# Kernel optimization log

Hardware: AMD Instinct MI355X
Metric: run time of the kernel (lower is better)

## Reference

```python
import jax, jax.numpy as jnp
import numpy as np

C = 256; G = 8; K = 3; P = K * K; GC = C // G
PAD = K // 2; PAD_DW = 1
EPS_LN = 1e-5; EPS_DWLN = 1e-6; EPS_BN = 1e-5
OFFSET_SCALE = 1.0


def _ln(x, g, b, eps=EPS_LN):
    mu = x.mean(-1, keepdims=True)
    var = ((x - mu) ** 2).mean(-1, keepdims=True)
    return (x - mu) * jax.lax.rsqrt(var + eps) * g + b


def _bn(x, g, b, m, v):  # x: NCHW, eval-mode batchnorm with running stats
    s = jax.lax.rsqrt(v + EPS_BN)
    return (x - m[None, :, None, None]) * (g * s)[None, :, None, None] + b[None, :, None, None]


def _dcnv3_core(x, offset, mask):
    # x: (N,H,W,C) projected input; offset: (N,H,W,G*P*2); mask: (N,H,W,G,P) softmaxed
    N, H, W, _ = x.shape
    Hp, Wp = H + 2 * PAD, W + 2 * PAD
    x_pad = jnp.pad(x, ((0, 0), (PAD, PAD), (PAD, PAD), (0, 0)))
    img = x_pad.reshape(N, Hp, Wp, G, GC).transpose(0, 3, 4, 1, 2)  # (N,G,gc,Hp,Wp)
    # reference points, normalized by padded spatial dims (stride=1, dilation=1)
    start = (K - 1) // 2 + 0.5
    ref_x = (start + jnp.arange(W, dtype=x.dtype)) / Wp
    ref_y = (start + jnp.arange(H, dtype=x.dtype)) / Hp
    rx, ry = jnp.meshgrid(ref_x, ref_y, indexing='xy')  # (H,W)
    ref = jnp.stack([rx, ry], -1)  # (H,W,2) as (x,y)
    # dilation grid (kernel tap offsets), tap index p = i_w*K + j_h per torch meshgrid order
    gw = (jnp.arange(K, dtype=x.dtype) - (K - 1) // 2) / Wp
    gh = (jnp.arange(K, dtype=x.dtype) - (K - 1) // 2) / Hp
    gxx, gyy = jnp.meshgrid(gw, gh, indexing='ij')
    grid = jnp.stack([gxx, gyy], -1).reshape(P, 2)
    norm = jnp.array([Wp, Hp], dtype=x.dtype)
    off = offset.reshape(N, H, W, G, P, 2) * (OFFSET_SCALE / norm)
    loc = ref[None, :, :, None, None, :] + grid * OFFSET_SCALE + off  # (N,H,W,G,P,2)
    sg = (2.0 * loc - 1.0).transpose(0, 3, 1, 2, 4, 5).reshape(N, G, H * W, P, 2)

    def sample_one(im, gr):  # im: (gc,Hp,Wp), gr: (HW,P,2) in [-1,1]
        gx = (gr[..., 0] + 1.0) * (Wp / 2) - 0.5  # align_corners=False
        gy = (gr[..., 1] + 1.0) * (Hp / 2) - 0.5
        x0 = jnp.floor(gx); y0 = jnp.floor(gy)
        wx = gx - x0; wy = gy - y0
        def gat(ix, iy):
            valid = ((ix >= 0) & (ix <= Wp - 1) & (iy >= 0) & (iy <= Hp - 1)).astype(im.dtype)
            ixc = jnp.clip(ix, 0, Wp - 1).astype(jnp.int32)
            iyc = jnp.clip(iy, 0, Hp - 1).astype(jnp.int32)
            return im[:, iyc, ixc] * valid  # (gc,HW,P), zero padding outside
        return (gat(x0, y0) * ((1 - wx) * (1 - wy))
                + gat(x0 + 1, y0) * (wx * (1 - wy))
                + gat(x0, y0 + 1) * ((1 - wx) * wy)
                + gat(x0 + 1, y0 + 1) * (wx * wy))

    sampled = jax.vmap(jax.vmap(sample_one))(img, sg)  # (N,G,gc,HW,P)
    m = mask.transpose(0, 3, 1, 2, 4).reshape(N, G, 1, H * W, P)
    out = (sampled * m).sum(-1)  # (N,G,gc,HW)
    return out.transpose(0, 3, 1, 2).reshape(N, H, W, C)


def _dcnv3(inp, dw_w, dw_b, dwln_g, dwln_b, off_w, off_b, msk_w, msk_b, inp_w, inp_b, outp_w, outp_b):
    N, H, W, _ = inp.shape
    x = inp @ inp_w + inp_b  # input_proj
    # depthwise conv offset/mask branch (on the raw input, not the projection)
    x1 = jax.lax.conv_general_dilated(inp, dw_w, (1, 1), ((PAD_DW, PAD_DW), (PAD_DW, PAD_DW)),
                                      dimension_numbers=('NHWC', 'HWIO', 'NHWC'),
                                      feature_group_count=C) + dw_b
    x1 = jax.nn.gelu(_ln(x1, dwln_g, dwln_b, EPS_DWLN), approximate=False)
    offset = x1 @ off_w + off_b  # (N,H,W,G*P*2)
    mask = jax.nn.softmax((x1 @ msk_w + msk_b).reshape(N, H, W, G, P), axis=-1)
    return _dcnv3_core(x, offset, mask) @ outp_w + outp_b  # output_proj


def _forward(x, conv1_w, bn1_g, bn1_b, bn1_m, bn1_v, ln1_g, ln1_b, dw_w, dw_b, dwln_g, dwln_b,
             off_w, off_b, msk_w, msk_b, inp_w, inp_b, outp_w, outp_b, gamma1,
             ln2_g, ln2_b, fc1_w, fc1_b, fc2_w, fc2_b, gamma2, bn2_g, bn2_b, bn2_m, bn2_v):
    out = jax.lax.conv_general_dilated(x, conv1_w, (1, 1), ((1, 1), (1, 1)),
                                       dimension_numbers=('NCHW', 'OIHW', 'NCHW'))
    out = jax.nn.relu(_bn(out, bn1_g, bn1_b, bn1_m, bn1_v))
    t = out.transpose(0, 2, 3, 1)  # NHWC for the InternImage layer
    # post_norm InternImage layer with layer_scale
    d = _dcnv3(t, dw_w, dw_b, dwln_g, dwln_b, off_w, off_b, msk_w, msk_b, inp_w, inp_b, outp_w, outp_b)
    t = t + gamma1 * _ln(d, ln1_g, ln1_b)
    h = jax.nn.gelu(t @ fc1_w + fc1_b, approximate=False) @ fc2_w + fc2_b
    t = t + gamma2 * _ln(h, ln2_g, ln2_b)
    out = _bn(t.transpose(0, 3, 1, 2), bn2_g, bn2_b, bn2_m, bn2_v)
    return jax.nn.relu(out + x)  # residual (downsample is None: stride=1, inplanes==planes)


def setup_inputs() -> dict:
    key = jax.random.key(0)
    ks = iter(jax.random.split(key, 48))
    rn = lambda shape, s=1.0: jax.random.normal(next(ks), shape, dtype=jnp.float32) * s
    hid = 4 * C
    d = {}
    d['x'] = rn((8, C, 56, 56))
    d['conv1_w'] = rn((C, C, 3, 3), (2.0 / (9 * C)) ** 0.5)
    d['bn1_g'] = jnp.ones((C,), jnp.float32); d['bn1_b'] = jnp.zeros((C,), jnp.float32)
    d['bn1_m'] = rn((C,), 0.1)
    d['bn1_v'] = jax.random.uniform(next(ks), (C,), jnp.float32, 0.5, 1.5)
    d['ln1_g'] = jnp.ones((C,), jnp.float32); d['ln1_b'] = jnp.zeros((C,), jnp.float32)
    d['dw_w'] = rn((3, 3, 1, C), (1.0 / 9) ** 0.5); d['dw_b'] = jnp.zeros((C,), jnp.float32)
    d['dwln_g'] = jnp.ones((C,), jnp.float32); d['dwln_b'] = jnp.zeros((C,), jnp.float32)
    d['off_w'] = rn((C, G * P * 2), 0.01); d['off_b'] = rn((G * P * 2,), 0.01)
    d['msk_w'] = rn((C, G * P), 0.01); d['msk_b'] = jnp.zeros((G * P,), jnp.float32)
    d['inp_w'] = rn((C, C), C ** -0.5); d['inp_b'] = jnp.zeros((C,), jnp.float32)
    d['outp_w'] = rn((C, C), C ** -0.5); d['outp_b'] = jnp.zeros((C,), jnp.float32)
    d['gamma1'] = rn((C,), 0.01)
    d['ln2_g'] = jnp.ones((C,), jnp.float32); d['ln2_b'] = jnp.zeros((C,), jnp.float32)
    d['fc1_w'] = rn((C, hid), C ** -0.5); d['fc1_b'] = jnp.zeros((hid,), jnp.float32)
    d['fc2_w'] = rn((hid, C), hid ** -0.5); d['fc2_b'] = jnp.zeros((C,), jnp.float32)
    d['gamma2'] = rn((C,), 0.01)
    d['bn2_g'] = jnp.ones((C,), jnp.float32); d['bn2_b'] = jnp.zeros((C,), jnp.float32)
    d['bn2_m'] = rn((C,), 0.1)
    d['bn2_v'] = jax.random.uniform(next(ks), (C,), jnp.float32, 0.5, 1.5)
    return d


def reference(x, conv1_w, bn1_g, bn1_b, bn1_m, bn1_v, ln1_g, ln1_b, dw_w, dw_b, dwln_g, dwln_b,
              off_w, off_b, msk_w, msk_b, inp_w, inp_b, outp_w, outp_b, gamma1,
              ln2_g, ln2_b, fc1_w, fc1_b, fc2_w, fc2_b, gamma2, bn2_g, bn2_b, bn2_m, bn2_v):
    return _forward(x, conv1_w, bn1_g, bn1_b, bn1_m, bn1_v, ln1_g, ln1_b, dw_w, dw_b, dwln_g, dwln_b,
                    off_w, off_b, msk_w, msk_b, inp_w, inp_b, outp_w, outp_b, gamma1,
                    ln2_g, ln2_b, fc1_w, fc1_b, fc2_w, fc2_b, gamma2, bn2_g, bn2_b, bn2_m, bn2_v)
```

## Files before the change

### kernel.cpp

```cpp
#include <hip/hip_runtime.h>
#include <cmath>

#define N_   8
#define H_   56
#define W_   56
#define C_   256
#define HW_  3136
#define NHW_ 25088
#define G_   8
#define GC_  32
#define P_   9
#define HID_ 1024
#define XP_H 58
#define XP_W 58

typedef __attribute__((ext_vector_type(8))) short bf16x8;
typedef __attribute__((ext_vector_type(4))) float f32x4;

#define GLOAD_LDS16(g, l) __builtin_amdgcn_global_load_lds( \
    (const __attribute__((address_space(1))) void*)(g), \
    (__attribute__((address_space(3))) void*)(l), 16, 0, 0)

__device__ __forceinline__ unsigned short f2bf(float f) {
    unsigned u = __float_as_uint(f);
    u += 0x7FFF + ((u >> 16) & 1);
    return (unsigned short)(u >> 16);
}

__device__ __forceinline__ float gelu_exact(float v) {
    return 0.5f * v * (1.f + erff(v * 0.70710678118654752f));
}

__device__ __forceinline__ float2 block_sum2(float a, float b, float* sm) {
    int lane = threadIdx.x & 63;
    int wid  = threadIdx.x >> 6;
#pragma unroll
    for (int off = 32; off > 0; off >>= 1) {
        a += __shfl_down(a, off, 64);
        b += __shfl_down(b, off, 64);
    }
    if (lane == 0) { sm[wid] = a; sm[wid + 4] = b; }
    __syncthreads();
    float ra = sm[0] + sm[1] + sm[2] + sm[3];
    float rb = sm[4] + sm[5] + sm[6] + sm[7];
    __syncthreads();
    return make_float2(ra, rb);
}

__global__ __launch_bounds__(256) void k_prep_xpad(const float* __restrict__ x, unsigned short* __restrict__ xpad) {
    int nh = blockIdx.x;
    int n = nh / H_, h = nh - n * H_;
    int c = threadIdx.x;
    const float* xr = x + ((size_t)(n * C_ + c)) * HW_ + h * W_;
    unsigned short* orow = xpad + ((size_t)((n * XP_H + h + 1) * XP_W + 1)) * C_ + c;
    for (int w = 0; w < W_; ++w) orow[(size_t)w * C_] = f2bf(xr[w]);
}

__global__ __launch_bounds__(256) void k_prep_wTT(const float* __restrict__ w, unsigned short* __restrict__ wTT) {
    int i  = blockIdx.x * 256 + threadIdx.x;
    int ci = i & 255;
    int r  = i >> 8;
    int co = r & 255;
    int kk = r >> 8;
    wTT[i] = f2bf(w[(co * 256 + ci) * 9 + kk]);
}

__global__ __launch_bounds__(256) void k_prep_sqT(const float* __restrict__ src, unsigned short* __restrict__ dst) {
    int n = blockIdx.x, k = threadIdx.x;
    dst[n * C_ + k] = f2bf(src[k * C_ + n]);
}

__global__ __launch_bounds__(256) void k_prep_fc1T(const float* __restrict__ src, unsigned short* __restrict__ dst) {
    int n = blockIdx.x, k = threadIdx.x;
    dst[(size_t)n * C_ + k] = f2bf(src[(size_t)k * HID_ + n]);
}

__global__ __launch_bounds__(256) void k_prep_fc2T(const float* __restrict__ src, unsigned short* __restrict__ dst) {
    int n = blockIdx.x, k0 = threadIdx.x;
#pragma unroll
    for (int q = 0; q < 4; ++q) {
        int k = q * 256 + k0;
        dst[(size_t)n * HID_ + k] = f2bf(src[(size_t)k * C_ + n]);
    }
}

__global__ __launch_bounds__(256) void k_prep_om(const float* __restrict__ offw, const float* __restrict__ offb,
                                                 const float* __restrict__ mskw, const float* __restrict__ mskb,
                                                 unsigned short* __restrict__ omT, float* __restrict__ omb) {
    int n = blockIdx.x, k = threadIdx.x;
    float v = 0.f;
    if (n < 144)      v = offw[k * 144 + n];
    else if (n < 216) v = mskw[k * 72 + (n - 144)];
    omT[n * C_ + k] = f2bf(v);
    if (k == 0) omb[n] = (n < 144) ? offb[n] : (n < 216 ? mskb[n - 144] : 0.f);
}

__global__ __launch_bounds__(256) void k_conv1_mfma(const unsigned short* __restrict__ xpad,
                                                    const unsigned short* __restrict__ wTT,
                                                    const float* __restrict__ g, const float* __restrict__ b,
                                                    const float* __restrict__ m, const float* __restrict__ v,
                                                    float* __restrict__ t, unsigned short* __restrict__ t_bf) {
    __shared__ __align__(16) unsigned char smem[49152];
    unsigned short* sm16 = (unsigned short*)smem;
    int tid = threadIdx.x;
    int wave = tid >> 6, lane = tid & 63;
    int r = lane & 15, kq = lane >> 4;
    int bid = blockIdx.x;
    int swz = (bid & 7) * 98 + (bid >> 3);
    int mt = swz >> 1, nt = swz & 1;
    int m0 = mt * 64, n0 = nt * 128;
    int wm = wave & 1, wn = wave >> 1;

    int pix = m0 + wave * 16 + r;
    int n = pix / HW_, hw = pix - n * HW_;
    int h = hw / W_, w = hw - h * W_;
    size_t abase = ((size_t)((n * XP_H + h) * XP_W + w)) * C_;

    f32x4 acc[2][4] = {};

    auto stage = [&](int kt, int buf) {
        int tap = kt >> 2, ktk = kt & 3;
        int kh = tap / 3, kw = tap - kh * 3;
        int k0 = ktk * 64;
        unsigned short* dstA = sm16 + buf * 12288;
        unsigned short* dstB = dstA + 4096;
        const unsigned short* ap = xpad + abase + (size_t)(kh * XP_W + kw) * C_ + k0;
#pragma unroll
        for (int i = 0; i < 2; ++i)
            GLOAD_LDS16(ap + (i * 4 + kq) * 8, dstA + (wave * 2 + i) * 512);
#pragma unroll
        for (int i = 0; i < 4; ++i) {
            int q = wave * 4 + i;
            int nrow = n0 + (q >> 1) * 16 + r;
            int cc   = (q & 1) * 4 + kq;
            GLOAD_LDS16(wTT + ((size_t)(tap * C_) + nrow) * C_ + k0 + cc * 8, dstB + q * 512);
        }
    };

    stage(0, 0);
    int cur = 0;
#pragma unroll 1
    for (int kt = 0; kt < 36; ++kt) {
        if (kt < 35) {
            stage(kt + 1, cur ^ 1);
            asm volatile("s_waitcnt vmcnt(6)" ::: "memory");
        } else {
            asm volatile("s_waitcnt vmcnt(0)" ::: "memory");
        }
        __builtin_amdgcn_s_barrier();
        bf16x8* sA = (bf16x8*)(sm16 + cur * 12288);
        bf16x8* sB = sA + 512;
#pragma unroll
        for (int ks = 0; ks < 2; ++ks) {
            bf16x8 af[2], bfr[4];
#pragma unroll
            for (int mi = 0; mi < 2; ++mi) af[mi]  = sA[((wm * 2 + mi) * 2 + ks) * 64 + lane];
#pragma unroll
            for (int ni = 0; ni < 4; ++ni) bfr[ni] = sB[((wn * 4 + ni) * 2 + ks) * 64 + lane];
#pragma unroll
            for (int mi = 0; mi < 2; ++mi)
#pragma unroll
                for (int ni = 0; ni < 4; ++ni)
                    acc[mi][ni] = __builtin_amdgcn_mfma_f32_16x16x32_bf16(af[mi], bfr[ni], acc[mi][ni], 0, 0, 0);
        }
        __builtin_amdgcn_s_barrier();
        cur ^= 1;
    }

#pragma unroll
    for (int ni = 0; ni < 4; ++ni) {
        int co = n0 + (wn * 4 + ni) * 16 + r;
        float sc = g[co] * rsqrtf(v[co] + 1e-5f);
        float sh = b[co] - m[co] * sc;
#pragma unroll
        for (int mi = 0; mi < 2; ++mi) {
#pragma unroll
            for (int reg = 0; reg < 4; ++reg) {
                int po = m0 + (wm * 2 + mi) * 16 + kq * 4 + reg;
                float val = fmaxf(acc[mi][ni][reg] * sc + sh, 0.f);
                size_t idx = (size_t)po * C_ + co;
                t[idx] = val;
                t_bf[idx] = f2bf(val);
            }
        }
    }
}

__global__ __launch_bounds__(256) void k_inproj_mfma(const unsigned short* __restrict__ t_bf,
                                                     const unsigned short* __restrict__ inpwT,
                                                     const float* __restrict__ bias,
                                                     float* __restrict__ xproj) {
    __shared__ __align__(16) unsigned char smem[81920];
    unsigned short* sm16 = (unsigned short*)smem;
    int tid = threadIdx.x;
    int wave = tid >> 6, lane = tid & 63;
    int r = lane & 15, kq = lane >> 4;
    int m0 = blockIdx.x * 64;

    f32x4 acc[16] = {};

    auto stage = [&](int kt, int buf) {
        int k0 = kt * 64;
        unsigned short* dstA = sm16 + buf * 20480;
        unsigned short* dstB = dstA + 4096;
#pragma unroll
        for (int i = 0; i < 2; ++i) {
            int q = wave * 2 + i;
            int row = m0 + wave * 16 + r;
            GLOAD_LDS16(t_bf + (size_t)row * C_ + k0 + (i * 4 + kq) * 8, dstA + q * 512);
        }
#pragma unroll
        for (int i = 0; i < 8; ++i) {
            int q = wave * 8 + i;
            int nrow = (q >> 1) * 16 + r;
            int cc   = (q & 1) * 4 + kq;
            GLOAD_LDS16(inpwT + (size_t)nrow * C_ + k0 + cc * 8, dstB + q * 512);
        }
    };

    stage(0, 0);
    int cur = 0;
#pragma unroll 1
    for (int kt = 0; kt < 4; ++kt) {
        if (kt < 3) {
            stage(kt + 1, cur ^ 1);
            asm volatile("s_waitcnt vmcnt(10)" ::: "memory");
        } else {
            asm volatile("s_waitcnt vmcnt(0)" ::: "memory");
        }
        __builtin_amdgcn_s_barrier();
        bf16x8* sA = (bf16x8*)(sm16 + cur * 20480);
        bf16x8* sB = sA + 512;
#pragma unroll
        for (int ks = 0; ks < 2; ++ks) {
            bf16x8 a = sA[(wave * 2 + ks) * 64 + lane];
#pragma unroll
            for (int ni = 0; ni < 16; ++ni) {
                bf16x8 b = sB[(ni * 2 + ks) * 64 + lane];
                acc[ni] = __builtin_amdgcn_mfma_f32_16x16x32_bf16(a, b, acc[ni], 0, 0, 0);
            }
        }
        __builtin_amdgcn_s_barrier();
        cur ^= 1;
    }

#pragma unroll
    for (int ni = 0; ni < 16; ++ni) {
        int col = ni * 16 + r;
        float bb = bias[col];
#pragma unroll
        for (int reg = 0; reg < 4; ++reg) {
            int row = m0 + wave * 16 + kq * 4 + reg;
            xproj[(size_t)row * C_ + col] = acc[ni][reg] + bb;
        }
    }
}

__global__ __launch_bounds__(256) void k_dw(const float* __restrict__ t, const float* __restrict__ dww,
                                            const float* __restrict__ dwb, const float* __restrict__ lg,
                                            const float* __restrict__ lb, unsigned short* __restrict__ x1_bf) {
    __shared__ float sm[8];
    int pix = blockIdx.x;
    int n = pix / HW_, hw = pix - n * HW_;
    int h = hw / W_,  w = hw - h * W_;
    int c = threadIdx.x;
    float acc = dwb[c];
#pragma unroll
    for (int kh = 0; kh < 3; ++kh) {
        int y = h + kh - 1;
        if ((unsigned)y >= H_) continue;
#pragma unroll
        for (int kw = 0; kw < 3; ++kw) {
            int xx = w + kw - 1;
            if ((unsigned)xx >= W_) continue;
            acc = fmaf(t[(size_t)(n * HW_ + y * W_ + xx) * C_ + c], dww[(kh * 3 + kw) * C_ + c], acc);
        }
    }
    float2 r  = block_sum2(acc, acc * acc, sm);
    float mu  = r.x * (1.f / C_);
    float var = fmaxf(r.y * (1.f / C_) - mu * mu, 0.f);
    float rs  = rsqrtf(var + 1e-6f);
    float val = (acc - mu) * rs * lg[c] + lb[c];
    x1_bf[(size_t)pix * C_ + c] = f2bf(gelu_exact(val));
}

__global__ __launch_bounds__(256) void k_offmask_mfma(const unsigned short* __restrict__ x1_bf,
                                                      const unsigned short* __restrict__ omT,
                                                      const float* __restrict__ omb,
                                                      float* __restrict__ offo, float* __restrict__ msko) {
    __shared__ float som[32][225];
    int wave = threadIdx.x >> 6, lane = threadIdx.x & 63;
    int r = lane & 15, kq = lane >> 4;
    int p0 = blockIdx.x * 32, co0 = wave * 64;
    f32x4 acc[2][4] = {};
#pragma unroll 1
    for (int ks = 0; ks < 8; ++ks) {
        bf16x8 a0 = *(const bf16x8*)(x1_bf + (size_t)(p0 + r) * C_ + ks * 32 + kq * 8);
        bf16x8 a1 = *(const bf16x8*)(x1_bf + (size_t)(p0 + 16 + r) * C_ + ks * 32 + kq * 8);
        const unsigned short* bp = omT + (size_t)(co0 + r) * C_ + ks * 32 + kq * 8;
#pragma unroll
        for (int ni = 0; ni < 4; ++ni) {
            bf16x8 b = *(const bf16x8*)(bp + (size_t)ni * 16 * C_);
            acc[0][ni] = __builtin_amdgcn_mfma_f32_16x16x32_bf16(a0, b, acc[0][ni], 0, 0, 0);
            acc[1][ni] = __builtin_amdgcn_mfma_f32_16x16x32_bf16(a1, b, acc[1][ni], 0, 0, 0);
        }
    }
#pragma unroll
    for (int ni = 0; ni < 4; ++ni) {
        int col = co0 + ni * 16 + r;
        if (col < 216) {
            float bb = omb[col];
#pragma unroll
            for (int mi = 0; mi < 2; ++mi)
#pragma unroll
                for (int reg = 0; reg < 4; ++reg)
                    som[mi * 16 + kq * 4 + reg][col] = acc[mi][ni][reg] + bb;
        }
    }
    __syncthreads();
    int tid = threadIdx.x;
#pragma unroll
    for (int i = 0; i < 18; ++i) {
        int j = i * 256 + tid;
        int px = j / 144, col = j - px * 144;
        offo[(size_t)(p0 + px) * 144 + col] = som[px][col];
    }
    int px = tid >> 3, g = tid & 7;
    float mx = -1e30f;
#pragma unroll
    for (int p = 0; p < 9; ++p) mx = fmaxf(mx, som[px][144 + g * 9 + p]);
    float e[9], s = 0.f;
#pragma unroll
    for (int p = 0; p < 9; ++p) { e[p] = expf(som[px][144 + g * 9 + p] - mx); s += e[p]; }
    float inv = 1.f / s;
#pragma unroll
    for (int p = 0; p < 9; ++p) msko[(size_t)(p0 + px) * 72 + g * 9 + p] = e[p] * inv;
}

__global__ __launch_bounds__(256) void k_core(const float* __restrict__ xp,
                                              const float* __restrict__ offo, const float* __restrict__ msko,
                                              unsigned short* __restrict__ core_bf) {
    int pix = blockIdx.x;
    int n = pix / HW_, hw = pix - n * HW_;
    int h = hw / W_,  w = hw - h * W_;
    int g  = threadIdx.x >> 5;
    int cc = threadIdx.x & 31;
    const float* op = offo + (size_t)pix * 144 + g * 18;
    const float* mp = msko + (size_t)pix * 72 + g * 9;
    const float* xg = xp + (size_t)n * HW_ * C_ + g * GC_ + cc;
    float acc = 0.f;
#pragma unroll
    for (int p = 0; p < 9; ++p) {
        float gx = (float)(w + (p / 3)) + op[p * 2];
        float gy = (float)(h + (p % 3)) + op[p * 2 + 1];
        float fx = floorf(gx), fy = floorf(gy);
        float wx = gx - fx,   wy = gy - fy;
        int ix = (int)fx - 1, iy = (int)fy - 1;
        float v00 = 0.f, v10 = 0.f, v01 = 0.f, v11 = 0.f;
        bool x0ok = (unsigned)ix < W_, x1ok = (unsigned)(ix + 1) < W_;
        bool y0ok = (unsigned)iy < H_, y1ok = (unsigned)(iy + 1) < H_;
        if (y0ok) {
            const float* rr = xg + (size_t)(iy * W_) * C_;
            if (x0ok) v00 = rr[(size_t)ix * C_];
            if (x1ok) v10 = rr[(size_t)(ix + 1) * C_];
        }
        if (y1ok) {
            const float* rr = xg + (size_t)((iy + 1) * W_) * C_;
            if (x0ok) v01 = rr[(size_t)ix * C_];
            if (x1ok) v11 = rr[(size_t)(ix + 1) * C_];
        }
        float sval = (v00 * (1.f - wx) + v10 * wx) * (1.f - wy)
                   + (v01 * (1.f - wx) + v11 * wx) * wy;
        acc = fmaf(mp[p], sval, acc);
    }
    core_bf[(size_t)pix * C_ + threadIdx.x] = f2bf(acc);
}

__global__ __launch_bounds__(256) void k_outproj_mfma(const unsigned short* __restrict__ core_bf,
                                                      const unsigned short* __restrict__ outpwT,
                                                      const float* __restrict__ bo,
                                                      const float* __restrict__ g1, const float* __restrict__ lg,
                                                      const float* __restrict__ lb,
                                                      float* __restrict__ t, unsigned short* __restrict__ t_bf) {
    __shared__ float sd[32][260];
    int wave = threadIdx.x >> 6, lane = threadIdx.x & 63;
    int r = lane & 15, kq = lane >> 4;
    int p0 = blockIdx.x * 32, co0 = wave * 64;
    f32x4 acc[2][4] = {};
#pragma unroll 1
    for (int ks = 0; ks < 8; ++ks) {
        bf16x8 a0 = *(const bf16x8*)(core_bf + (size_t)(p0 + r) * C_ + ks * 32 + kq * 8);
        bf16x8 a1 = *(const bf16x8*)(core_bf + (size_t)(p0 + 16 + r) * C_ + ks * 32 + kq * 8);
        const unsigned short* bp = outpwT + (size_t)(co0 + r) * C_ + ks * 32 + kq * 8;
#pragma unroll
        for (int ni = 0; ni < 4; ++ni) {
            bf16x8 b = *(const bf16x8*)(bp + (size_t)ni * 16 * C_);
            acc[0][ni] = __builtin_amdgcn_mfma_f32_16x16x32_bf16(a0, b, acc[0][ni], 0, 0, 0);
            acc[1][ni] = __builtin_amdgcn_mfma_f32_16x16x32_bf16(a1, b, acc[1][ni], 0, 0, 0);
        }
    }
#pragma unroll
    for (int ni = 0; ni < 4; ++ni) {
        int col = co0 + ni * 16 + r;
        float bb = bo[col];
#pragma unroll
        for (int mi = 0; mi < 2; ++mi)
#pragma unroll
            for (int reg = 0; reg < 4; ++reg)
                sd[mi * 16 + kq * 4 + reg][col] = acc[mi][ni][reg] + bb;
    }
    __syncthreads();
    int px = threadIdx.x >> 3, sub = threadIdx.x & 7;
    float s1 = 0.f, s2 = 0.f;
#pragma unroll
    for (int i = 0; i < 8; ++i) {
        float4 vv = *(const float4*)&sd[px][sub * 32 + i * 4];
        s1 += vv.x + vv.y + vv.z + vv.w;
        s2 += vv.x * vv.x + vv.y * vv.y + vv.z * vv.z + vv.w * vv.w;
    }
#pragma unroll
    for (int off = 1; off < 8; off <<= 1) { s1 += __shfl_xor(s1, off, 64); s2 += __shfl_xor(s2, off, 64); }
    float mu  = s1 * (1.f / C_);
    float var = fmaxf(s2 * (1.f / C_) - mu * mu, 0.f);
    float rs  = rsqrtf(var + 1e-5f);
#pragma unroll
    for (int i = 0; i < 32; ++i) {
        int col = sub * 32 + i;
        size_t idx = (size_t)(p0 + px) * C_ + col;
        float tn = t[idx] + g1[col] * ((sd[px][col] - mu) * rs * lg[col] + lb[col]);
        t[idx] = tn;
        t_bf[idx] = f2bf(tn);
    }
}

__global__ __launch_bounds__(256) void k_fc1_mfma(const unsigned short* __restrict__ t_bf,
                                                  const unsigned short* __restrict__ fc1wT,
                                                  const float* __restrict__ fc1b,
                                                  unsigned short* __restrict__ h_bf) {
    __shared__ __align__(16) unsigned char smem[34816];
    unsigned short* sm16 = (unsigned short*)smem;
    bf16x8* sA = (bf16x8*)smem;
    bf16x8* sB = (bf16x8*)(smem + 16384);
    int tid = threadIdx.x;
    int wave = tid >> 6, lane = tid & 63;
    int r = lane & 15, kq = lane >> 4;
    int mt = blockIdx.x >> 3, nt = blockIdx.x & 7;
    int m0 = mt * 128, n0 = nt * 128;
    int wm = wave & 1, wn = wave >> 1;

    f32x4 acc[4][4] = {};
#pragma unroll 1
    for (int kt = 0; kt < 4; ++kt) {
        int k0 = kt * 64;
        if (kt) __syncthreads();
#pragma unroll
        for (int i = 0; i < 4; ++i) {
            int q = wave * 4 + i;
            int row = m0 + (q >> 1) * 16 + r;
            int cc  = (q & 1) * 4 + kq;
            GLOAD_LDS16(t_bf + (size_t)row * C_ + k0 + cc * 8, sm16 + q * 512);
        }
#pragma unroll
        for (int i = 0; i < 4; ++i) {
            int q = wave * 4 + i;
            int nrow = n0 + (q >> 1) * 16 + r;
            int cc   = (q & 1) * 4 + kq;
            GLOAD_LDS16(fc1wT + (size_t)nrow * C_ + k0 + cc * 8, sm16 + 8192 + q * 512);
        }
        __syncthreads();
#pragma unroll
        for (int ks = 0; ks < 2; ++ks) {
            bf16x8 af[4], bfr[4];
#pragma unroll
            for (int mi = 0; mi < 4; ++mi) af[mi]  = sA[((wm * 4 + mi) * 2 + ks) * 64 + lane];
#pragma unroll
            for (int ni = 0; ni < 4; ++ni) bfr[ni] = sB[((wn * 4 + ni) * 2 + ks) * 64 + lane];
#pragma unroll
            for (int mi = 0; mi < 4; ++mi)
#pragma unroll
                for (int ni = 0; ni < 4; ++ni)
                    acc[mi][ni] = __builtin_amdgcn_mfma_f32_16x16x32_bf16(af[mi], bfr[ni], acc[mi][ni], 0, 0, 0);
        }
    }
    __syncthreads();
#pragma unroll
    for (int ni = 0; ni < 4; ++ni) {
        int col = (wn * 4 + ni) * 16 + r;
        float bb = fc1b[n0 + col];
#pragma unroll
        for (int mi = 0; mi < 4; ++mi)
#pragma unroll
            for (int reg = 0; reg < 4; ++reg) {
                int row = (wm * 4 + mi) * 16 + kq * 4 + reg;
                sm16[row * 136 + col] = f2bf(gelu_exact(acc[mi][ni][reg] + bb));
            }
    }
    __syncthreads();
    int trow = tid >> 1, thalf = tid & 1;
    const unsigned short* src = sm16 + trow * 136 + thalf * 64;
    unsigned short* dst = h_bf + (size_t)(m0 + trow) * HID_ + n0 + thalf * 64;
#pragma unroll
    for (int j = 0; j < 8; ++j)
        *(bf16x8*)(dst + j * 8) = *(const bf16x8*)(src + j * 8);
}

__global__ __launch_bounds__(256) void k_fc2fin_mfma(const unsigned short* __restrict__ h_bf,
                                                     const unsigned short* __restrict__ fc2wT,
                                                     const float* __restrict__ fc2b,
                                                     const float* __restrict__ g2, const float* __restrict__ lg,
                                                     const float* __restrict__ lb, const float* __restrict__ t,
                                                     const float* __restrict__ x,
                                                     const float* __restrict__ bn2g, const float* __restrict__ bn2b,
                                                     const float* __restrict__ bn2m, const float* __restrict__ bn2v,
                                                     float* __restrict__ out) {
    __shared__ __align__(16) unsigned char smem[81920];
    unsigned short* sm16 = (unsigned short*)smem;
    int tid = threadIdx.x;
    int wave = tid >> 6, lane = tid & 63;
    int r = lane & 15, kq = lane >> 4;
    int m0 = blockIdx.x * 64;

    f32x4 acc[16] = {};

    auto stage = [&](int kt, int buf) {
        int k0 = kt * 64;
        unsigned short* dstA = sm16 + buf * 20480;
        unsigned short* dstB = dstA + 4096;
#pragma unroll
        for (int i = 0; i < 2; ++i) {
            int q = wave * 2 + i;
            int row = m0 + wave * 16 + r;
            GLOAD_LDS16(h_bf + (size_t)row * HID_ + k0 + (i * 4 + kq) * 8, dstA + q * 512);
        }
#pragma unroll
        for (int i = 0; i < 8; ++i) {
            int q = wave * 8 + i;
            int nrow = (q >> 1) * 16 + r;
            int cc   = (q & 1) * 4 + kq;
            GLOAD_LDS16(fc2wT + (size_t)nrow * HID_ + k0 + cc * 8, dstB + q * 512);
        }
    };

    stage(0, 0);
    int cur = 0;
#pragma unroll 1
    for (int kt = 0; kt < 16; ++kt) {
        if (kt < 15) {
            stage(kt + 1, cur ^ 1);
            asm volatile("s_waitcnt vmcnt(10)" ::: "memory");
        } else {
            asm volatile("s_waitcnt vmcnt(0)" ::: "memory");
        }
        __builtin_amdgcn_s_barrier();
        bf16x8* sA = (bf16x8*)(sm16 + cur * 20480);
        bf16x8* sB = sA + 512;
#pragma unroll
        for (int ks = 0; ks < 2; ++ks) {
            bf16x8 a = sA[(wave * 2 + ks) * 64 + lane];
#pragma unroll
            for (int ni = 0; ni < 16; ++ni) {
                bf16x8 b = sB[(ni * 2 + ks) * 64 + lane];
                acc[ni] = __builtin_amdgcn_mfma_f32_16x16x32_bf16(a, b, acc[ni], 0, 0, 0);
            }
        }
        __builtin_amdgcn_s_barrier();
        cur ^= 1;
    }

    float* ot = (float*)smem;
    float bb[16], g2v[16], lgv[16], lbv[16];
#pragma unroll
    for (int ni = 0; ni < 16; ++ni) {
        int col = ni * 16 + r;
        bb[ni] = fc2b[col]; g2v[ni] = g2[col]; lgv[ni] = lg[col]; lbv[ni] = lb[col];
    }
#pragma unroll
    for (int ni = 0; ni < 16; ++ni)
#pragma unroll
        for (int reg = 0; reg < 4; ++reg) acc[ni][reg] += bb[ni];
#pragma unroll
    for (int reg = 0; reg < 4; ++reg) {
        float s1 = 0.f, s2 = 0.f;
#pragma unroll
        for (int ni = 0; ni < 16; ++ni) { float vv = acc[ni][reg]; s1 += vv; s2 += vv * vv; }
#pragma unroll
        for (int off = 1; off < 16; off <<= 1) { s1 += __shfl_xor(s1, off, 64); s2 += __shfl_xor(s2, off, 64); }
        float mu  = s1 * (1.f / C_);
        float var = fmaxf(s2 * (1.f / C_) - mu * mu, 0.f);
        float rs  = rsqrtf(var + 1e-5f);
        int row_local = wave * 16 + kq * 4 + reg;
        const float* tr = t + (size_t)(m0 + row_local) * C_;
#pragma unroll
        for (int ni = 0; ni < 16; ++ni) {
            int col = ni * 16 + r;
            ot[row_local * 257 + col] = tr[col] + g2v[ni] * ((acc[ni][reg] - mu) * rs * lgv[ni] + lbv[ni]);
        }
    }
    __syncthreads();

    int n  = m0 / HW_;
    int hw0 = m0 - n * HW_;
#pragma unroll 1
    for (int i = 0; i < 64; ++i) {
        int c = wave * 64 + i;
        float sc = bn2g[c] * rsqrtf(bn2v[c] + 1e-5f);
        float sh = bn2b[c] - bn2m[c] * sc;
        size_t gidx = ((size_t)(n * C_ + c)) * HW_ + hw0 + lane;
        float val = ot[lane * 257 + c] * sc + sh + x[gidx];
        out[gidx] = fmaxf(val, 0.f);
    }
}

extern "C" void kernel_launch(void* const* d_in, const int* in_sizes, int n_in,
                              void* d_out, int out_size, void* d_ws, size_t ws_size,
                              hipStream_t stream) {
    const float* x      = (const float*)d_in[0];
    const float* conv1w = (const float*)d_in[1];
    const float* bn1g   = (const float*)d_in[2];
    const float* bn1b   = (const float*)d_in[3];
    const float* bn1m   = (const float*)d_in[4];
    const float* bn1v   = (const float*)d_in[5];
    const float* ln1g   = (const float*)d_in[6];
    const float* ln1b   = (const float*)d_in[7];
    const float* dww    = (const float*)d_in[8];
    const float* dwb    = (const float*)d_in[9];
    const float* dwlng  = (const float*)d_in[10];
    const float* dwlnb  = (const float*)d_in[11];
    const float* offw   = (const float*)d_in[12];
    const float* offb   = (const float*)d_in[13];
    const float* mskw   = (const float*)d_in[14];
    const float* mskb   = (const float*)d_in[15];
    const float* inpw   = (const float*)d_in[16];
    const float* inpb   = (const float*)d_in[17];
    const float* outpw  = (const float*)d_in[18];
    const float* outpb  = (const float*)d_in[19];
    const float* gamma1 = (const float*)d_in[20];
    const float* ln2g   = (const float*)d_in[21];
    const float* ln2b   = (const float*)d_in[22];
    const float* fc1w   = (const float*)d_in[23];
    const float* fc1b   = (const float*)d_in[24];
    const float* fc2w   = (const float*)d_in[25];
    const float* fc2b   = (const float*)d_in[26];
    const float* gamma2 = (const float*)d_in[27];
    const float* bn2g   = (const float*)d_in[28];
    const float* bn2b   = (const float*)d_in[29];
    const float* bn2m   = (const float*)d_in[30];
    const float* bn2v   = (const float*)d_in[31];
    float* out = (float*)d_out;

    float* ws    = (float*)d_ws;
    float* xproj = ws;
    float* offo  = xproj + (size_t)NHW_ * C_;
    float* msko  = offo  + (size_t)NHW_ * 144;
    unsigned short* x1_bf = (unsigned short*)(msko + (size_t)NHW_ * 72);
    unsigned short* scr   = x1_bf + (size_t)NHW_ * C_;
    float* t     = (float*)(scr + (size_t)N_ * XP_H * XP_W * C_);
    float* omb   = t + (size_t)NHW_ * C_;
    unsigned short* t_bf  = (unsigned short*)(omb + 256);
    unsigned short* wTT   = t_bf  + (size_t)NHW_ * C_;
    unsigned short* inpwT = wTT   + (size_t)9 * C_ * C_;
    unsigned short* outpwT= inpwT + (size_t)C_ * C_;
    unsigned short* fc1wT = outpwT+ (size_t)C_ * C_;
    unsigned short* fc2wT = fc1wT + (size_t)HID_ * C_;
    unsigned short* omT   = fc2wT + (size_t)C_ * HID_;
    unsigned short* xpad    = scr;
    unsigned short* core_bf = scr;
    unsigned short* h_bf    = (unsigned short*)xproj;

    hipMemsetAsync(xpad, 0, (size_t)N_ * XP_H * XP_W * C_ * sizeof(unsigned short), stream);
    k_prep_xpad<<<N_ * H_, 256, 0, stream>>>(x, xpad);
    k_prep_wTT <<<2304,    256, 0, stream>>>(conv1w, wTT);
    k_prep_sqT <<<256,     256, 0, stream>>>(inpw, inpwT);
    k_prep_sqT <<<256,     256, 0, stream>>>(outpw, outpwT);
    k_prep_fc1T<<<1024,    256, 0, stream>>>(fc1w, fc1wT);
    k_prep_fc2T<<<256,     256, 0, stream>>>(fc2w, fc2wT);
    k_prep_om  <<<256,     256, 0, stream>>>(offw, offb, mskw, mskb, omT, omb);

    k_conv1_mfma  <<<(NHW_ / 64) * 2, 256, 0, stream>>>(xpad, wTT, bn1g, bn1b, bn1m, bn1v, t, t_bf);
    k_inproj_mfma <<<NHW_ / 64, 256, 0, stream>>>(t_bf, inpwT, inpb, xproj);
    k_dw          <<<NHW_,      256, 0, stream>>>(t, dww, dwb, dwlng, dwlnb, x1_bf);
    k_offmask_mfma<<<NHW_ / 32, 256, 0, stream>>>(x1_bf, omT, omb, offo, msko);
    k_core        <<<NHW_,      256, 0, stream>>>(xproj, offo, msko, core_bf);
    k_outproj_mfma<<<NHW_ / 32, 256, 0, stream>>>(core_bf, outpwT, outpb, gamma1, ln1g, ln1b, t, t_bf);
    k_fc1_mfma    <<<(NHW_ / 128) * 8, 256, 0, stream>>>(t_bf, fc1wT, fc1b, h_bf);
    k_fc2fin_mfma <<<NHW_ / 64, 256, 0, stream>>>(h_bf, fc2wT, fc2b, gamma2, ln2g, ln2b, t,
                                                  x, bn2g, bn2b, bn2m, bn2v, out);
}
```

Baseline: 625.0 us.

## Enlarge conv1 tile, store xproj in bf16, and batch depthwise conv per block

The conv1 GEMM tile grows from 64 to 128 output pixels with a K-step of 32, so each B-tile load is reused across more rows. The in-projection output is stored as bf16 and the deformable sampling kernel reads bf16, which halves its gather traffic. The depthwise conv now reads the bf16 copy of t and processes four pixels per block, reusing a 3x6 neighbourhood held in registers. The workspace is rearranged so h_bf and xproj_bf alias. Bf16 storage of xproj lowers precision, and the smaller K-step doubles the number of barriers per tile.

```diff
diff --git a/kernel.cpp b/kernel.cpp
--- a/kernel.cpp
+++ b/kernel.cpp
@@ -27,6 +27,10 @@
     return (unsigned short)(u >> 16);
 }
 
+__device__ __forceinline__ float bf2f(unsigned short u) {
+    return __uint_as_float((unsigned)u << 16);
+}
+
 __device__ __forceinline__ float gelu_exact(float v) {
     return 0.5f * v * (1.f + erff(v * 0.70710678118654752f));
 }
@@ -100,69 +104,71 @@
                                                     const float* __restrict__ g, const float* __restrict__ b,
                                                     const float* __restrict__ m, const float* __restrict__ v,
                                                     float* __restrict__ t, unsigned short* __restrict__ t_bf) {
-    __shared__ __align__(16) unsigned char smem[49152];
+    __shared__ __align__(16) unsigned char smem[32768];
     unsigned short* sm16 = (unsigned short*)smem;
     int tid = threadIdx.x;
     int wave = tid >> 6, lane = tid & 63;
     int r = lane & 15, kq = lane >> 4;
     int bid = blockIdx.x;
-    int swz = (bid & 7) * 98 + (bid >> 3);
+    int swz = (bid & 7) * 49 + (bid >> 3);
     int mt = swz >> 1, nt = swz & 1;
-    int m0 = mt * 64, n0 = nt * 128;
+    int m0 = mt * 128, n0 = nt * 128;
     int wm = wave & 1, wn = wave >> 1;
 
-    int pix = m0 + wave * 16 + r;
-    int n = pix / HW_, hw = pix - n * HW_;
-    int h = hw / W_, w = hw - h * W_;
-    size_t abase = ((size_t)((n * XP_H + h) * XP_W + w)) * C_;
-
-    f32x4 acc[2][4] = {};
+    size_t abase[2];
+#pragma unroll
+    for (int i = 0; i < 2; ++i) {
+        int pix = m0 + (wave * 2 + i) * 16 + r;
+        int n = pix / HW_, hw = pix - n * HW_;
+        int h = hw / W_, w = hw - h * W_;
+        abase[i] = ((size_t)((n * XP_H + h) * XP_W + w)) * C_ + kq * 8;
+    }
+
+    f32x4 acc[4][4] = {};
 
     auto stage = [&](int kt, int buf) {
-        int tap = kt >> 2, ktk = kt & 3;
+        int tap = kt >> 3, ktk = kt & 7;
         int kh = tap / 3, kw = tap - kh * 3;
-        int k0 = ktk * 64;
-        unsigned short* dstA = sm16 + buf * 12288;
+        int k0 = ktk * 32;
+        unsigned short* dstA = sm16 + buf * 8192;
         unsigned short* dstB = dstA + 4096;
-        const unsigned short* ap = xpad + abase + (size_t)(kh * XP_W + kw) * C_ + k0;
-#pragma unroll
-        for (int i = 0; i < 2; ++i)
-            GLOAD_LDS16(ap + (i * 4 + kq) * 8, dstA + (wave * 2 + i) * 512);
-#pragma unroll
-        for (int i = 0; i < 4; ++i) {
-            int q = wave * 4 + i;
-            int nrow = n0 + (q >> 1) * 16 + r;
-            int cc   = (q & 1) * 4 + kq;
-            GLOAD_LDS16(wTT + ((size_t)(tap * C_) + nrow) * C_ + k0 + cc * 8, dstB + q * 512);
+        size_t aoff = (size_t)(kh * XP_W + kw) * C_ + k0;
+#pragma unroll
+        for (int i = 0; i < 2; ++i) {
+            int q = wave * 2 + i;
+            GLOAD_LDS16(xpad + abase[i] + aoff, dstA + q * 512);
+        }
+#pragma unroll
+        for (int i = 0; i < 2; ++i) {
+            int q = wave * 2 + i;
+            int nrow = n0 + q * 16 + r;
+            GLOAD_LDS16(wTT + ((size_t)(tap * C_) + nrow) * C_ + k0 + kq * 8, dstB + q * 512);
         }
     };
 
     stage(0, 0);
     int cur = 0;
 #pragma unroll 1
-    for (int kt = 0; kt < 36; ++kt) {
-        if (kt < 35) {
+    for (int kt = 0; kt < 72; ++kt) {
+        if (kt < 71) {
             stage(kt + 1, cur ^ 1);
-            asm volatile("s_waitcnt vmcnt(6)" ::: "memory");
+            asm volatile("s_waitcnt vmcnt(4)" ::: "memory");
         } else {
             asm volatile("s_waitcnt vmcnt(0)" ::: "memory");
         }
         __builtin_amdgcn_s_barrier();
-        bf16x8* sA = (bf16x8*)(sm16 + cur * 12288);
+        bf16x8* sA = (bf16x8*)(sm16 + cur * 8192);
         bf16x8* sB = sA + 512;
-#pragma unroll
-        for (int ks = 0; ks < 2; ++ks) {
-            bf16x8 af[2], bfr[4];
-#pragma unroll
-            for (int mi = 0; mi < 2; ++mi) af[mi]  = sA[((wm * 2 + mi) * 2 + ks) * 64 + lane];
-#pragma unroll
-            for (int ni = 0; ni < 4; ++ni) bfr[ni] = sB[((wn * 4 + ni) * 2 + ks) * 64 + lane];
-#pragma unroll
-            for (int mi = 0; mi < 2; ++mi)
-#pragma unroll
-                for (int ni = 0; ni < 4; ++ni)
-                    acc[mi][ni] = __builtin_amdgcn_mfma_f32_16x16x32_bf16(af[mi], bfr[ni], acc[mi][ni], 0, 0, 0);
-        }
+        bf16x8 af[4], bfr[4];
+#pragma unroll
+        for (int mi = 0; mi < 4; ++mi) af[mi]  = sA[(wm * 4 + mi) * 64 + lane];
+#pragma unroll
+        for (int ni = 0; ni < 4; ++ni) bfr[ni] = sB[(wn * 4 + ni) * 64 + lane];
+#pragma unroll
+        for (int mi = 0; mi < 4; ++mi)
+#pragma unroll
+            for (int ni = 0; ni < 4; ++ni)
+                acc[mi][ni] = __builtin_amdgcn_mfma_f32_16x16x32_bf16(af[mi], bfr[ni], acc[mi][ni], 0, 0, 0);
         __builtin_amdgcn_s_barrier();
         cur ^= 1;
     }
@@ -173,10 +179,10 @@
         float sc = g[co] * rsqrtf(v[co] + 1e-5f);
         float sh = b[co] - m[co] * sc;
 #pragma unroll
-        for (int mi = 0; mi < 2; ++mi) {
+        for (int mi = 0; mi < 4; ++mi) {
 #pragma unroll
             for (int reg = 0; reg < 4; ++reg) {
-                int po = m0 + (wm * 2 + mi) * 16 + kq * 4 + reg;
+                int po = m0 + (wm * 4 + mi) * 16 + kq * 4 + reg;
                 float val = fmaxf(acc[mi][ni][reg] * sc + sh, 0.f);
                 size_t idx = (size_t)po * C_ + co;
                 t[idx] = val;
@@ -189,7 +195,7 @@
 __global__ __launch_bounds__(256) void k_inproj_mfma(const unsigned short* __restrict__ t_bf,
                                                      const unsigned short* __restrict__ inpwT,
                                                      const float* __restrict__ bias,
-                                                     float* __restrict__ xproj) {
+                                                     unsigned short* __restrict__ xproj_bf) {
     __shared__ __align__(16) unsigned char smem[81920];
     unsigned short* sm16 = (unsigned short*)smem;
     int tid = threadIdx.x;
@@ -251,37 +257,52 @@
 #pragma unroll
         for (int reg = 0; reg < 4; ++reg) {
             int row = m0 + wave * 16 + kq * 4 + reg;
-            xproj[(size_t)row * C_ + col] = acc[ni][reg] + bb;
-        }
-    }
-}
-
-__global__ __launch_bounds__(256) void k_dw(const float* __restrict__ t, const float* __restrict__ dww,
+            xproj_bf[(size_t)row * C_ + col] = f2bf(acc[ni][reg] + bb);
+        }
+    }
+}
+
+__global__ __launch_bounds__(256) void k_dw(const unsigned short* __restrict__ t_bf, const float* __restrict__ dww,
                                             const float* __restrict__ dwb, const float* __restrict__ lg,
                                             const float* __restrict__ lb, unsigned short* __restrict__ x1_bf) {
     __shared__ float sm[8];
-    int pix = blockIdx.x;
-    int n = pix / HW_, hw = pix - n * HW_;
-    int h = hw / W_,  w = hw - h * W_;
+    int p0 = blockIdx.x * 4;
+    int n = p0 / HW_, hw = p0 - n * HW_;
+    int h = hw / W_, w0 = hw - h * W_;
     int c = threadIdx.x;
-    float acc = dwb[c];
-#pragma unroll
-    for (int kh = 0; kh < 3; ++kh) {
-        int y = h + kh - 1;
-        if ((unsigned)y >= H_) continue;
-#pragma unroll
-        for (int kw = 0; kw < 3; ++kw) {
-            int xx = w + kw - 1;
-            if ((unsigned)xx >= W_) continue;
-            acc = fmaf(t[(size_t)(n * HW_ + y * W_ + xx) * C_ + c], dww[(kh * 3 + kw) * C_ + c], acc);
-        }
-    }
-    float2 r  = block_sum2(acc, acc * acc, sm);
-    float mu  = r.x * (1.f / C_);
-    float var = fmaxf(r.y * (1.f / C_) - mu * mu, 0.f);
-    float rs  = rsqrtf(var + 1e-6f);
-    float val = (acc - mu) * rs * lg[c] + lb[c];
-    x1_bf[(size_t)pix * C_ + c] = f2bf(gelu_exact(val));
+
+    float vals[3][6];
+#pragma unroll
+    for (int dy = 0; dy < 3; ++dy) {
+        int y = h + dy - 1;
+        bool rowok = (unsigned)y < H_;
+#pragma unroll
+        for (int dx = 0; dx < 6; ++dx) {
+            int xx = w0 + dx - 1;
+            bool ok = rowok && ((unsigned)xx < W_);
+            vals[dy][dx] = ok ? bf2f(t_bf[((size_t)(n * HW_ + y * W_ + xx)) * C_ + c]) : 0.f;
+        }
+    }
+    float wv[9];
+#pragma unroll
+    for (int k = 0; k < 9; ++k) wv[k] = dww[k * C_ + c];
+    float bias = dwb[c], lgc = lg[c], lbc = lb[c];
+
+#pragma unroll 1
+    for (int px = 0; px < 4; ++px) {
+        float acc = bias;
+#pragma unroll
+        for (int kh = 0; kh < 3; ++kh)
+#pragma unroll
+            for (int kw = 0; kw < 3; ++kw)
+                acc = fmaf(vals[kh][px + kw], wv[kh * 3 + kw], acc);
+        float2 rr = block_sum2(acc, acc * acc, sm);
+        float mu  = rr.x * (1.f / C_);
+        float var = fmaxf(rr.y * (1.f / C_) - mu * mu, 0.f);
+        float rs  = rsqrtf(var + 1e-6f);
+        float val = (acc - mu) * rs * lgc + lbc;
+        x1_bf[(size_t)(p0 + px) * C_ + c] = f2bf(gelu_exact(val));
+    }
 }
 
 __global__ __launch_bounds__(256) void k_offmask_mfma(const unsigned short* __restrict__ x1_bf,
@@ -337,7 +358,7 @@
     for (int p = 0; p < 9; ++p) msko[(size_t)(p0 + px) * 72 + g * 9 + p] = e[p] * inv;
 }
 
-__global__ __launch_bounds__(256) void k_core(const float* __restrict__ xp,
+__global__ __launch_bounds__(256) void k_core(const unsigned short* __restrict__ xp,
                                               const float* __restrict__ offo, const float* __restrict__ msko,
                                               unsigned short* __restrict__ core_bf) {
     int pix = blockIdx.x;
@@ -347,7 +368,7 @@
     int cc = threadIdx.x & 31;
     const float* op = offo + (size_t)pix * 144 + g * 18;
     const float* mp = msko + (size_t)pix * 72 + g * 9;
-    const float* xg = xp + (size_t)n * HW_ * C_ + g * GC_ + cc;
+    const unsigned short* xg = xp + (size_t)n * HW_ * C_ + g * GC_ + cc;
     float acc = 0.f;
 #pragma unroll
     for (int p = 0; p < 9; ++p) {
@@ -360,14 +381,14 @@
         bool x0ok = (unsigned)ix < W_, x1ok = (unsigned)(ix + 1) < W_;
         bool y0ok = (unsigned)iy < H_, y1ok = (unsigned)(iy + 1) < H_;
         if (y0ok) {
-            const float* rr = xg + (size_t)(iy * W_) * C_;
-            if (x0ok) v00 = rr[(size_t)ix * C_];
-            if (x1ok) v10 = rr[(size_t)(ix + 1) * C_];
+            const unsigned short* rr = xg + (size_t)(iy * W_) * C_;
+            if (x0ok) v00 = bf2f(rr[(size_t)ix * C_]);
+            if (x1ok) v10 = bf2f(rr[(size_t)(ix + 1) * C_]);
         }
         if (y1ok) {
-            const float* rr = xg + (size_t)((iy + 1) * W_) * C_;
-            if (x0ok) v01 = rr[(size_t)ix * C_];
-            if (x1ok) v11 = rr[(size_t)(ix + 1) * C_];
+            const unsigned short* rr = xg + (size_t)((iy + 1) * W_) * C_;
+            if (x0ok) v01 = bf2f(rr[(size_t)ix * C_]);
+            if (x1ok) v11 = bf2f(rr[(size_t)(ix + 1) * C_]);
         }
         float sval = (v00 * (1.f - wx) + v10 * wx) * (1.f - wy)
                    + (v01 * (1.f - wx) + v11 * wx) * wy;
@@ -648,12 +669,12 @@
     const float* bn2v   = (const float*)d_in[31];
     float* out = (float*)d_out;
 
-    float* ws    = (float*)d_ws;
-    float* xproj = ws;
-    float* offo  = xproj + (size_t)NHW_ * C_;
-    float* msko  = offo  + (size_t)NHW_ * 144;
+    unsigned short* h_bf     = (unsigned short*)d_ws;
+    unsigned short* xproj_bf = (unsigned short*)d_ws;
+    float* offo  = (float*)(xproj_bf + (size_t)NHW_ * C_);
+    float* msko  = offo + (size_t)NHW_ * 144;
     unsigned short* x1_bf = (unsigned short*)(msko + (size_t)NHW_ * 72);
-    unsigned short* scr   = x1_bf + (size_t)NHW_ * C_;
+    unsigned short* scr   = h_bf + (size_t)NHW_ * HID_;
     float* t     = (float*)(scr + (size_t)N_ * XP_H * XP_W * C_);
     float* omb   = t + (size_t)NHW_ * C_;
     unsigned short* t_bf  = (unsigned short*)(omb + 256);
@@ -665,7 +686,6 @@
     unsigned short* omT   = fc2wT + (size_t)C_ * HID_;
     unsigned short* xpad    = scr;
     unsigned short* core_bf = scr;
-    unsigned short* h_bf    = (unsigned short*)xproj;
 
     hipMemsetAsync(xpad, 0, (size_t)N_ * XP_H * XP_W * C_ * sizeof(unsigned short), stream);
     k_prep_xpad<<<N_ * H_, 256, 0, stream>>>(x, xpad);
@@ -676,11 +696,11 @@
     k_prep_fc2T<<<256,     256, 0, stream>>>(fc2w, fc2wT);
     k_prep_om  <<<256,     256, 0, stream>>>(offw, offb, mskw, mskb, omT, omb);
 
-    k_conv1_mfma  <<<(NHW_ / 64) * 2, 256, 0, stream>>>(xpad, wTT, bn1g, bn1b, bn1m, bn1v, t, t_bf);
-    k_inproj_mfma <<<NHW_ / 64, 256, 0, stream>>>(t_bf, inpwT, inpb, xproj);
-    k_dw          <<<NHW_,      256, 0, stream>>>(t, dww, dwb, dwlng, dwlnb, x1_bf);
+    k_conv1_mfma  <<<(NHW_ / 128) * 2, 256, 0, stream>>>(xpad, wTT, bn1g, bn1b, bn1m, bn1v, t, t_bf);
+    k_inproj_mfma <<<NHW_ / 64, 256, 0, stream>>>(t_bf, inpwT, inpb, xproj_bf);
+    k_dw          <<<NHW_ / 4,  256, 0, stream>>>(t_bf, dww, dwb, dwlng, dwlnb, x1_bf);
     k_offmask_mfma<<<NHW_ / 32, 256, 0, stream>>>(x1_bf, omT, omb, offo, msko);
-    k_core        <<<NHW_,      256, 0, stream>>>(xproj, offo, msko, core_bf);
+    k_core        <<<NHW_,      256, 0, stream>>>(xproj_bf, offo, msko, core_bf);
     k_outproj_mfma<<<NHW_ / 32, 256, 0, stream>>>(core_bf, outpwT, outpb, gamma1, ln1g, ln1b, t, t_bf);
     k_fc1_mfma    <<<(NHW_ / 128) * 8, 256, 0, stream>>>(t_bf, fc1wT, fc1b, h_bf);
     k_fc2fin_mfma <<<NHW_ / 64, 256, 0, stream>>>(h_bf, fc2wT, fc2b, gamma2, ln2g, ln2b, t,
```

New measurement: 707.9 us. 1.13x slower.
